# Performance work log

Measured on AMD Instinct MI355X. Metric: run time of the kernel, lower is better.

Reference implementation:

```python
import jax, jax.numpy as jnp
from jax import lax
import numpy as np

DN = ('NCDHW', 'OIDHW', 'NCDHW')
EPS = 1e-3  # BatchNorm1d eps=0.001
GRID = (41, 512, 512)  # spatial_shape [40,512,512] + [1,0,0]


def _block(x, mask, w, gamma, beta, rmean, rvar, stride, padding):
    # Regular (non-submanifold) sparse conv computes the same values as a dense
    # conv on the zero-filled grid; active OUTPUT sites are exactly those reached
    # by any active input site through the kernel window. BN+ReLU act only on
    # active sites (inactive sites stay exactly 0), hence the mask multiply.
    y = lax.conv_general_dilated(x, w, stride, padding, dimension_numbers=DN)
    k1 = jnp.ones((1, 1) + w.shape[2:], x.dtype)
    m = lax.conv_general_dilated(mask, k1, stride, padding, dimension_numbers=DN)
    m = (m > 0).astype(x.dtype)
    inv = gamma / jnp.sqrt(rvar + EPS)
    scale = inv.reshape(1, -1, 1, 1, 1)
    shift = (beta - rmean * inv).reshape(1, -1, 1, 1, 1)
    return jax.nn.relu(y * scale + shift) * m, m


def setup_inputs() -> dict:
    key = jax.random.key(0)
    NV, B = 120000, 2
    kf, kb, kz, ky, kx, kp = jax.random.split(key, 6)
    voxel_features = jax.random.normal(kf, (NV, 3), jnp.float32)
    coors = jnp.stack([
        jax.random.randint(kb, (NV,), 0, B, jnp.int32),
        jax.random.randint(kz, (NV,), 0, 40, jnp.int32),
        jax.random.randint(ky, (NV,), 0, 512, jnp.int32),
        jax.random.randint(kx, (NV,), 0, 512, jnp.int32)], axis=1)
    inp = {"voxel_features": voxel_features, "coors": coors, "batch_size": B}
    chans = [(3, 16, (3, 3, 3)), (16, 32, (3, 3, 3)), (32, 64, (3, 3, 3)), (64, 64, (3, 1, 1))]
    for i, (ci, co, k) in enumerate(chans, 1):
        kw, kg, kbb, km, kv = jax.random.split(jax.random.fold_in(kp, i), 5)
        fan = ci * k[0] * k[1] * k[2]
        inp[f"w{i}"] = jax.random.normal(kw, (co, ci) + k, jnp.float32) / np.sqrt(fan).astype(np.float32)
        inp[f"g{i}"] = jax.random.uniform(kg, (co,), jnp.float32, 0.5, 1.5)
        inp[f"bb{i}"] = jax.random.normal(kbb, (co,), jnp.float32) * 0.1
        inp[f"rm{i}"] = jax.random.normal(km, (co,), jnp.float32) * 0.1
        inp[f"rv{i}"] = jax.random.uniform(kv, (co,), jnp.float32, 0.5, 1.5)
    return inp


def reference(voxel_features, coors, batch_size,
              w1, g1, bb1, rm1, rv1,
              w2, g2, bb2, rm2, rv2,
              w3, g3, bb3, rm3, rv3,
              w4, g4, bb4, rm4, rv4):
    D, H, W = GRID
    C = voxel_features.shape[1]
    b, z, y, x = coors[:, 0], coors[:, 1], coors[:, 2], coors[:, 3]
    dense = jnp.zeros((batch_size, C, D, H, W), voxel_features.dtype)
    dense = dense.at[b, :, z, y, x].add(voxel_features)  # scatter voxels to grid
    mask = jnp.zeros((batch_size, 1, D, H, W), voxel_features.dtype).at[b, 0, z, y, x].set(1.0)
    h, m = _block(dense, mask, w1, g1, bb1, rm1, rv1, (2, 2, 2), [(1, 1), (1, 1), (1, 1)])
    h, m = _block(h, m, w2, g2, bb2, rm2, rv2, (2, 2, 2), [(1, 1), (1, 1), (1, 1)])
    h, m = _block(h, m, w3, g3, bb3, rm3, rv3, (2, 2, 2), [(0, 0), (1, 1), (1, 1)])
    h, m = _block(h, m, w4, g4, bb4, rm4, rv4, (2, 1, 1), [(0, 0), (0, 0), (0, 0)])
    N, Co, Dd, Hh, Ww = h.shape  # [B, 64, 2, 64, 64]
    return h.reshape(N, Co * Dd, Hh, Ww)
```

## Files before the change

kernel.cpp:

```cpp
#include <hip/hip_runtime.h>

#define EPS 1e-3f


static __device__ __forceinline__ unsigned f2bf(float f) {
    unsigned u = __float_as_uint(f);
    return (u + 0x7FFFu + ((u >> 16) & 1u)) >> 16;
}

typedef _Float16 f16x8 __attribute__((ext_vector_type(8)));
typedef float f32x4 __attribute__((ext_vector_type(4)));
typedef float f32x16 __attribute__((ext_vector_type(16)));

__global__ __launch_bounds__(256) void repack(
    const float* __restrict__ g1, const float* __restrict__ b1,
    const float* __restrict__ rm1, const float* __restrict__ rv1,
    const float* __restrict__ w2, const float* __restrict__ g2, const float* __restrict__ b2,
    const float* __restrict__ rm2, const float* __restrict__ rv2,
    const float* __restrict__ w3, const float* __restrict__ g3, const float* __restrict__ b3,
    const float* __restrict__ rm3, const float* __restrict__ rv3,
    const float* __restrict__ w4, const float* __restrict__ g4, const float* __restrict__ b4,
    const float* __restrict__ rm4, const float* __restrict__ rv4,
    _Float16* __restrict__ wB2, _Float16* __restrict__ wB3,
    _Float16* __restrict__ wB4, float* __restrict__ shb)
{
    const int i = blockIdx.x * 256 + threadIdx.x;
    if (i < 13824) {
        const int j = i & 7, lane = (i >> 3) & 63, tap = i >> 9;
        const int oc = lane & 31;
        const int cin = (lane >> 5) * 8 + j;
        const float inv = g2[oc] * rsqrtf(rv2[oc] + EPS);
        wB2[i] = (_Float16)(w2[(oc * 16 + cin) * 27 + tap] * inv);
    } else if (i >= 14336 && i < 69632) {
        const int j2 = i - 14336;
        const int j = j2 & 7, lane = (j2 >> 3) & 63, t = (j2 >> 9) & 3, tap = j2 >> 11;
        const int q = lane >> 4, n = lane & 15;
        const int oc = t * 16 + n;
        const int cin = q * 8 + j;
        const float inv = g3[oc] * rsqrtf(rv3[oc] + EPS);
        wB3[j2] = (_Float16)(w3[(oc * 32 + cin) * 27 + tap] * inv);
    } else if (i >= 69632 && i < 81920) {
        const int j2 = i - 69632;
        const int j = j2 & 7, lane = (j2 >> 3) & 63, t = (j2 >> 9) & 3, c = j2 >> 11;
        const int q = lane >> 4, n = lane & 15;
        const int oc = t * 16 + n;
        const int k = c * 32 + q * 8 + j;
        const int dz = k >> 6, cin = k & 63;
        const float inv = g4[oc] * rsqrtf(rv4[oc] + EPS);
        wB4[j2] = (_Float16)(w4[(oc * 64 + cin) * 3 + dz] * inv);
    } else if (i >= 81920 && i < 82112) {
        const int j = i - 81920;
        if (j < 32) {
            const float inv = g2[j] * rsqrtf(rv2[j] + EPS);
            shb[j] = b2[j] - rm2[j] * inv;
        } else if (j < 96) {
            const int o = j - 32;
            const float inv = g3[o] * rsqrtf(rv3[o] + EPS);
            shb[j] = b3[o] - rm3[o] * inv;
        } else if (j < 160) {
            const int o = j - 96;
            const float inv = g4[o] * rsqrtf(rv4[o] + EPS);
            shb[j] = b4[o] - rm4[o] * inv;
        } else if (j < 176) {
            const int o = j - 160;
            shb[j] = g1[o] * rsqrtf(rv1[o] + EPS);
        } else if (j < 192) {
            const int o = j - 176;
            const float inv = g1[o] * rsqrtf(rv1[o] + EPS);
            shb[j] = b1[o] - rm1[o] * inv;
        }
    }
}

__global__ __launch_bounds__(256) void scatter_l1(
    const float* __restrict__ vf, const int* __restrict__ coors, int NV,
    const float* __restrict__ w1, unsigned short* __restrict__ y1,
    float* __restrict__ m1)
{
    __shared__ float ws[16 * 3 * 27];
    for (int e = threadIdx.x; e < 16 * 3 * 27; e += 256) ws[e] = w1[e];
    __syncthreads();

    const int gid = blockIdx.x * 256 + threadIdx.x;
    const int i = gid >> 3;
    const int oc2 = gid & 7;
    if (i >= NV) return;
    const int oc = oc2 * 2;

    const int b = coors[4 * i + 0];
    const int z = coors[4 * i + 1];
    const int y = coors[4 * i + 2];
    const int x = coors[4 * i + 3];
    const float f0 = vf[3 * i + 0];
    const float f1 = vf[3 * i + 1];
    const float f2 = vf[3 * i + 2];

    int ozv[2], kzv[2], nz = 0;
    int oyv[2], kyv[2], ny = 0;
    int oxv[2], kxv[2], nx = 0;
#pragma unroll
    for (int k = 0; k < 3; ++k) {
        int t = z + 1 - k;
        if (t >= 0 && !(t & 1)) { int o = t >> 1; if (o < 21) { ozv[nz] = o; kzv[nz] = k; ++nz; } }
    }
#pragma unroll
    for (int k = 0; k < 3; ++k) {
        int t = y + 1 - k;
        if (t >= 0 && !(t & 1)) { int o = t >> 1; if (o < 256) { oyv[ny] = o; kyv[ny] = k; ++ny; } }
    }
#pragma unroll
    for (int k = 0; k < 3; ++k) {
        int t = x + 1 - k;
        if (t >= 0 && !(t & 1)) { int o = t >> 1; if (o < 256) { oxv[nx] = o; kxv[nx] = k; ++nx; } }
    }

    for (int a = 0; a < nz; ++a)
        for (int bb = 0; bb < ny; ++bb)
            for (int c = 0; c < nx; ++c) {
                const int oz = ozv[a], oy = oyv[bb], ox = oxv[c];
                const int tap = (kzv[a] * 3 + kyv[bb]) * 3 + kxv[c];
                const int sp = oz * 65536 + oy * 256 + ox;
                if (oc2 == 0) m1[b * 1376256 + sp] = 1.0f;
                const float s0 = ws[oc * 81 + tap] * f0 + ws[oc * 81 + 27 + tap] * f1 +
                                 ws[oc * 81 + 54 + tap] * f2;
                const float s1 = ws[(oc + 1) * 81 + tap] * f0 +
                                 ws[(oc + 1) * 81 + 27 + tap] * f1 +
                                 ws[(oc + 1) * 81 + 54 + tap] * f2;
                const unsigned pk = f2bf(s0) | (f2bf(s1) << 16);
                unsigned* addr = (unsigned*)(y1 + (size_t)(b * 1376256 + sp) * 16 +
                                             oc2 * 2);
                asm volatile("global_atomic_pk_add_bf16 %0, %1, off"
                             : : "v"(addr), "v"(pk) : "memory");
            }
}

__global__ __launch_bounds__(256) void h1_pass(
    uint4* __restrict__ y1b, const float* __restrict__ m1,
    const float* __restrict__ shb, float* __restrict__ m2)
{
    const int idx = blockIdx.x * 256 + threadIdx.x;
    const float mv = m1[idx];
    uint4 u0 = y1b[idx * 2], u1 = y1b[idx * 2 + 1];
    const unsigned d[8] = {u0.x, u0.y, u0.z, u0.w, u1.x, u1.y, u1.z, u1.w};
    unsigned o[8];
#pragma unroll
    for (int j = 0; j < 8; ++j) {
        const int c0 = 2 * j;
        const float vlo = __uint_as_float(d[j] << 16);
        const float vhi = __uint_as_float(d[j] & 0xFFFF0000u);
        const float v0 = fmaxf(vlo * shb[160 + c0] + shb[176 + c0], 0.f) * mv;
        const float v1 = fmaxf(vhi * shb[160 + c0 + 1] + shb[176 + c0 + 1], 0.f) * mv;
        o[j] = __builtin_bit_cast(unsigned, __builtin_amdgcn_cvt_pkrtz(v0, v1));
    }
    uint4 w0, w1;
    w0.x = o[0]; w0.y = o[1]; w0.z = o[2]; w0.w = o[3];
    w1.x = o[4]; w1.y = o[5]; w1.z = o[6]; w1.w = o[7];
    y1b[idx * 2] = w0;
    y1b[idx * 2 + 1] = w1;

    if (idx < 360448) {
        const int b = idx / 180224;
        const int r = idx - b * 180224;
        const int oz = r >> 14, r2 = r & 16383, oy = r2 >> 7, ox = r2 & 127;
        const int iz0 = 2 * oz - 1, iyb = 2 * oy - 1, ixb = 2 * ox - 1;
        float msum = 0.f;
#pragma unroll
        for (int kz = 0; kz < 3; ++kz) {
            const int iz = iz0 + kz;
#pragma unroll
            for (int ky = 0; ky < 3; ++ky) {
                const int iy = iyb + ky;
#pragma unroll
                for (int kx = 0; kx < 3; ++kx) {
                    const int ix = ixb + kx;
                    if ((unsigned)iz < 21u && (unsigned)iy < 256u &&
                        (unsigned)ix < 256u)
                        msum += m1[b * 1376256 + iz * 65536 + iy * 256 + ix];
                }
            }
        }
        m2[idx] = msum > 0.f ? 1.f : 0.f;
    }
}

__global__ __launch_bounds__(256) void build_m3(
    const float* __restrict__ m2, float* __restrict__ m3)
{
    const int idx = blockIdx.x * 256 + threadIdx.x;
    if (idx >= 40960) return;
    const int b = idx / 20480;
    const int r = idx - b * 20480;
    const int oz = r >> 12, r2 = r & 4095, oy = r2 >> 6, ox = r2 & 63;
    const int iz0 = 2 * oz, iyb = 2 * oy - 1, ixb = 2 * ox - 1;

    float msum = 0.f;
#pragma unroll
    for (int kz = 0; kz < 3; ++kz) {
        const int iz = iz0 + kz;
#pragma unroll
        for (int ky = 0; ky < 3; ++ky) {
            const int iy = iyb + ky;
#pragma unroll
            for (int kx = 0; kx < 3; ++kx) {
                const int ix = ixb + kx;
                if ((unsigned)iy < 128u && (unsigned)ix < 128u)
                    msum += m2[b * 180224 + iz * 16384 + iy * 128 + ix];
            }
        }
    }
    m3[idx] = msum > 0.f ? 1.f : 0.f;
}

__global__ __launch_bounds__(256) __attribute__((amdgpu_waves_per_eu(4, 8)))
void conv_l2(
    const unsigned char* __restrict__ h1,
    const uint4* __restrict__ wB2,
    const float* __restrict__ m2, const float* __restrict__ shb,
    _Float16* __restrict__ h2h)
{
    const int tid = threadIdx.x;
    const int gw = blockIdx.x * 4 + (tid >> 6);
    const int lane = tid & 63;
    const int m = lane & 31, h = lane >> 5;

    const int plane = gw >> 9;
    const int rem = gw & 511;
    const int oy = rem >> 2;
    const int ox0 = (rem & 3) * 32;
    const int b = plane / 11, oz = plane % 11;
    const int iz0 = 2 * oz - 1, iyb = 2 * oy - 1;
    const int ixm = 2 * (ox0 + m) - 1;
    const int bbase = b * 1376256;
    const int qoff = h * 16;

    f32x16 acc;
#pragma unroll
    for (int r = 0; r < 16; ++r) acc[r] = 0.f;

    uint4 buf[13];
    bool  val[13];
#pragma unroll
    for (int t = 0; t < 13; ++t) {
        const int kz = t / 9, ky = (t / 3) % 3, kx = t % 3;
        const int iz = iz0 + kz, iy = iyb + ky, ix = ixm + kx;
        const bool v = (unsigned)iz < 21u && (unsigned)iy < 256u &&
                       (unsigned)ix < 256u;
        const int cell = bbase + iz * 65536 + iy * 256 + ix;
        buf[t] = *(const uint4*)(h1 + (v ? (cell * 32 + qoff) : 0));
        val[t] = v;
    }

#pragma unroll
    for (int tap = 0; tap < 27; ++tap) {
        const int s = tap % 13;
        uint4 ua = buf[s];
        if (!val[s]) { ua.x = 0; ua.y = 0; ua.z = 0; ua.w = 0; }
        if (tap + 13 < 27) {
            const int t2 = tap + 13;
            const int kz = t2 / 9, ky = (t2 / 3) % 3, kx = t2 % 3;
            const int iz = iz0 + kz, iy = iyb + ky, ix = ixm + kx;
            const bool v = (unsigned)iz < 21u && (unsigned)iy < 256u &&
                           (unsigned)ix < 256u;
            const int cell = bbase + iz * 65536 + iy * 256 + ix;
            buf[s] = *(const uint4*)(h1 + (v ? (cell * 32 + qoff) : 0));
            val[s] = v;
        }
        const f16x8 af = __builtin_bit_cast(f16x8, ua);
        const f16x8 bf = __builtin_bit_cast(f16x8, wB2[tap * 64 + lane]);
        acc = __builtin_amdgcn_mfma_f32_32x32x16_f16(af, bf, acc, 0, 0, 0);
    }

    const int oc = lane & 31;
#pragma unroll
    for (int r = 0; r < 16; ++r) {
        const int row = (r & 3) + 8 * (r >> 2) + 4 * h;
        const int px = ox0 + row;
        const int spo = oz * 16384 + oy * 128 + px;
        const float mv = m2[b * 180224 + spo];
        const size_t cbase = (size_t)(b * 180224 + spo) * 32;
        h2h[cbase + oc] = (_Float16)(fmaxf(acc[r] + shb[oc], 0.f) * mv);
    }
}

__global__ __launch_bounds__(256) __attribute__((amdgpu_waves_per_eu(4, 8)))
void conv_l3(
    const unsigned char* __restrict__ h2h,
    const uint4* __restrict__ wB3,
    const float* __restrict__ m3, const float* __restrict__ shb,
    _Float16* __restrict__ h3h)
{
    const int tid = threadIdx.x;
    const int gw = blockIdx.x * 4 + (tid >> 6);
    const int lane = tid & 63;
    const int m = lane & 15, q = lane >> 4;

    const int plane = gw >> 8;
    const int rem = gw & 255;
    const int oy = rem >> 2;
    const int ox0 = (rem & 3) * 16;
    const int b = plane / 5, oz = plane % 5;
    const int iz0 = 2 * oz, iyb = 2 * oy - 1;
    const int ixm = 2 * (ox0 + m) - 1;
    const int bbase = b * 180224;
    const int qoff = q * 16;

    f32x4 acc[4];
#pragma unroll
    for (int t = 0; t < 4; ++t) acc[t] = (f32x4){0.f, 0.f, 0.f, 0.f};

    uint4 buf[9];
    bool  val[9];
#pragma unroll
    for (int t = 0; t < 9; ++t) {
        const int ky = (t / 3) % 3, kx = t % 3;
        const int iz = iz0 + t / 9, iy = iyb + ky, ix = ixm + kx;
        const bool v = (unsigned)iy < 128u && (unsigned)ix < 128u;
        const int cell = bbase + iz * 16384 + iy * 128 + ix;
        buf[t] = *(const uint4*)(h2h + (v ? (cell * 64 + qoff) : 0));
        val[t] = v;
    }

#pragma unroll
    for (int tap = 0; tap < 27; ++tap) {
        const int s = tap % 9;
        uint4 ua = buf[s];
        if (!val[s]) { ua.x = 0; ua.y = 0; ua.z = 0; ua.w = 0; }
        if (tap + 9 < 27) {
            const int t2 = tap + 9;
            const int kz = t2 / 9, ky = (t2 / 3) % 3, kx = t2 % 3;
            const int iz = iz0 + kz, iy = iyb + ky, ix = ixm + kx;
            const bool v = (unsigned)iy < 128u && (unsigned)ix < 128u;
            const int cell = bbase + iz * 16384 + iy * 128 + ix;
            buf[s] = *(const uint4*)(h2h + (v ? (cell * 64 + qoff) : 0));
            val[s] = v;
        }
        const f16x8 af = __builtin_bit_cast(f16x8, ua);
#pragma unroll
        for (int t = 0; t < 4; ++t) {
            const f16x8 bf = __builtin_bit_cast(f16x8, wB3[(tap * 4 + t) * 64 + lane]);
            acc[t] = __builtin_amdgcn_mfma_f32_16x16x32_f16(af, bf, acc[t], 0, 0, 0);
        }
    }

    const int n = lane & 15;
#pragma unroll
    for (int r = 0; r < 4; ++r) {
        const int px = ox0 + q * 4 + r;
        const int spo = oz * 4096 + oy * 64 + px;
        const float mv = m3[b * 20480 + spo];
        const size_t cb = (size_t)(b * 20480 + spo) * 64;
#pragma unroll
        for (int t = 0; t < 4; ++t) {
            const int oc = t * 16 + n;
            h3h[cb + oc] = (_Float16)(fmaxf(acc[t][r] + shb[32 + oc], 0.f) * mv);
        }
    }
}

__global__ __launch_bounds__(256) __attribute__((amdgpu_waves_per_eu(4, 8)))
void conv_l4(
    const unsigned char* __restrict__ h3h,
    const uint4* __restrict__ wB4,
    const float* __restrict__ m3, const float* __restrict__ shb,
    float* __restrict__ out)
{
    const int tid = threadIdx.x;
    const int gw = blockIdx.x * 4 + (tid >> 6);
    const int lane = tid & 63;
    const int m = lane & 15, q = lane >> 4;

    const int b = gw >> 9, od = (gw >> 8) & 1;
    const int oy = (gw >> 2) & 63, ox0 = (gw & 3) * 16;
    const int cellbase = (b * 5 + 2 * od) * 4096 + oy * 64 + ox0 + m;

    f32x4 acc[4];
#pragma unroll
    for (int t = 0; t < 4; ++t) acc[t] = (f32x4){0.f, 0.f, 0.f, 0.f};

#pragma unroll
    for (int c = 0; c < 6; ++c) {
        const int dz = c >> 1;
        const size_t addr = (size_t)(cellbase + dz * 4096) * 128 +
                            (c & 1) * 64 + q * 16;
        const uint4 ua = *(const uint4*)(h3h + addr);
        const f16x8 af = __builtin_bit_cast(f16x8, ua);
#pragma unroll
        for (int t = 0; t < 4; ++t) {
            const f16x8 bf = __builtin_bit_cast(f16x8, wB4[(c * 4 + t) * 64 + lane]);
            acc[t] = __builtin_amdgcn_mfma_f32_16x16x32_f16(af, bf, acc[t], 0, 0, 0);
        }
    }

    const int n = lane & 15;
#pragma unroll
    for (int r = 0; r < 4; ++r) {
        const int px = ox0 + q * 4 + r;
        const int spo = oy * 64 + px;
        const float msum = m3[(b * 5 + 2 * od + 0) * 4096 + spo] +
                           m3[(b * 5 + 2 * od + 1) * 4096 + spo] +
                           m3[(b * 5 + 2 * od + 2) * 4096 + spo];
        const float mv = msum > 0.f ? 1.f : 0.f;
#pragma unroll
        for (int t = 0; t < 4; ++t) {
            const int oc = t * 16 + n;
            out[((b * 64 + oc) * 2 + od) * 4096 + spo] =
                fmaxf(acc[t][r] + shb[96 + oc], 0.f) * mv;
        }
    }
}

extern "C" void kernel_launch(void* const* d_in, const int* in_sizes, int n_in,
                              void* d_out, int out_size, void* d_ws, size_t ws_size,
                              hipStream_t stream)
{
    const float* vf    = (const float*)d_in[0];
    const int*   coors = (const int*)d_in[1];
    const float* w1 = (const float*)d_in[3];
    const float* g1 = (const float*)d_in[4];
    const float* b1 = (const float*)d_in[5];
    const float* rm1 = (const float*)d_in[6];
    const float* rv1 = (const float*)d_in[7];
    const float* w2 = (const float*)d_in[8];
    const float* g2 = (const float*)d_in[9];
    const float* b2 = (const float*)d_in[10];
    const float* rm2 = (const float*)d_in[11];
    const float* rv2 = (const float*)d_in[12];
    const float* w3 = (const float*)d_in[13];
    const float* g3 = (const float*)d_in[14];
    const float* b3 = (const float*)d_in[15];
    const float* rm3 = (const float*)d_in[16];
    const float* rv3 = (const float*)d_in[17];
    const float* w4 = (const float*)d_in[18];
    const float* g4 = (const float*)d_in[19];
    const float* b4 = (const float*)d_in[20];
    const float* rm4 = (const float*)d_in[21];
    const float* rv4 = (const float*)d_in[22];

    const int NV = in_sizes[0] / 3;

    float* ws = (float*)d_ws;
    float* y1  = ws;
    float* m1  = y1 + 22020096;
    float* h2h = m1 + 2752512;
    float* m2  = h2h + 5767168;
    float* h3h = m2 + 360448;
    float* m3  = h3h + 1310720;
    float* wB2 = m3 + 40960;
    float* wB3 = wB2 + 7168;
    float* wB4 = wB3 + 27648;
    float* shb = wB4 + 6144;

    (void)hipMemsetAsync(y1, 0, (size_t)(22020096 + 2752512) * sizeof(float), stream);

    repack<<<321, 256, 0, stream>>>(g1, b1, rm1, rv1,
                                    w2, g2, b2, rm2, rv2, w3, g3, b3, rm3, rv3,
                                    w4, g4, b4, rm4, rv4,
                                    (_Float16*)wB2, (_Float16*)wB3,
                                    (_Float16*)wB4, shb);
    scatter_l1<<<(NV * 8 + 255) / 256, 256, 0, stream>>>(vf, coors, NV, w1,
                                                         (unsigned short*)y1, m1);
    h1_pass<<<10752, 256, 0, stream>>>((uint4*)y1, m1, shb, m2);
    build_m3<<<160, 256, 0, stream>>>(m2, m3);
    conv_l2<<<2816, 256, 0, stream>>>((const unsigned char*)y1, (const uint4*)wB2,
                                      m2, shb, (_Float16*)h2h);
    conv_l3<<<640, 256, 0, stream>>>((const unsigned char*)h2h, (const uint4*)wB3,
                                     m3, shb, (_Float16*)h3h);
    conv_l4<<<256, 256, 0, stream>>>((const unsigned char*)h3h, (const uint4*)wB4,
                                     m3, shb, (float*)d_out);
}
```

Baseline: 238.3 us.

## Replace full-grid memset with sparse prezero and byte mask for layer one

```diff
diff --git a/kernel.cpp b/kernel.cpp
--- a/kernel.cpp
+++ b/kernel.cpp
@@ -12,7 +12,7 @@
 typedef float f32x4 __attribute__((ext_vector_type(4)));
 typedef float f32x16 __attribute__((ext_vector_type(16)));
 
-__global__ __launch_bounds__(256) void repack(
+__global__ __launch_bounds__(256) void repack_prezero(
     const float* __restrict__ g1, const float* __restrict__ b1,
     const float* __restrict__ rm1, const float* __restrict__ rv1,
     const float* __restrict__ w2, const float* __restrict__ g2, const float* __restrict__ b2,
@@ -22,8 +22,46 @@
     const float* __restrict__ w4, const float* __restrict__ g4, const float* __restrict__ b4,
     const float* __restrict__ rm4, const float* __restrict__ rv4,
     _Float16* __restrict__ wB2, _Float16* __restrict__ wB3,
-    _Float16* __restrict__ wB4, float* __restrict__ shb)
-{
+    _Float16* __restrict__ wB4, float* __restrict__ shb,
+    const int* __restrict__ coors, int NV, unsigned short* __restrict__ y1)
+{
+    if (blockIdx.x >= 321) {
+        const int i = (blockIdx.x - 321) * 256 + threadIdx.x;
+        if (i < NV) {
+            const int b = coors[4 * i + 0];
+            const int z = coors[4 * i + 1];
+            const int y = coors[4 * i + 2];
+            const int x = coors[4 * i + 3];
+            int ozv[2], nz = 0, oyv[2], ny = 0, oxv[2], nx = 0;
+#pragma unroll
+            for (int k = 0; k < 3; ++k) {
+                int t = z + 1 - k;
+                if (t >= 0 && !(t & 1)) { int o = t >> 1; if (o < 21) ozv[nz++] = o; }
+            }
+#pragma unroll
+            for (int k = 0; k < 3; ++k) {
+                int t = y + 1 - k;
+                if (t >= 0 && !(t & 1)) { int o = t >> 1; if (o < 256) oyv[ny++] = o; }
+            }
+#pragma unroll
+            for (int k = 0; k < 3; ++k) {
+                int t = x + 1 - k;
+                if (t >= 0 && !(t & 1)) { int o = t >> 1; if (o < 256) oxv[nx++] = o; }
+            }
+            const uint4 zz = {0u, 0u, 0u, 0u};
+            for (int a = 0; a < nz; ++a)
+                for (int bb = 0; bb < ny; ++bb)
+                    for (int c = 0; c < nx; ++c) {
+                        const int sp = ozv[a] * 65536 + oyv[bb] * 256 + oxv[c];
+                        uint4* p = (uint4*)(y1 + (size_t)(b * 1376256 + sp) * 16);
+                        p[0] = zz;
+                        p[1] = zz;
+                    }
+        }
+        asm volatile("s_waitcnt vmcnt(0)" ::: "memory");
+        return;
+    }
+
     const int i = blockIdx.x * 256 + threadIdx.x;
     if (i < 13824) {
         const int j = i & 7, lane = (i >> 3) & 63, tap = i >> 9;
@@ -74,96 +112,104 @@
 
 __global__ __launch_bounds__(256) void scatter_l1(
     const float* __restrict__ vf, const int* __restrict__ coors, int NV,
-    const float* __restrict__ w1, unsigned short* __restrict__ y1,
-    float* __restrict__ m1)
+    const float* __restrict__ w1, const float* __restrict__ shb,
+    unsigned short* __restrict__ y1, unsigned char* __restrict__ m1)
 {
     __shared__ float ws[16 * 3 * 27];
-    for (int e = threadIdx.x; e < 16 * 3 * 27; e += 256) ws[e] = w1[e];
+    for (int e = threadIdx.x; e < 16 * 3 * 27; e += 256)
+        ws[e] = w1[e] * shb[160 + e / 81];
     __syncthreads();
 
     const int gid = blockIdx.x * 256 + threadIdx.x;
     const int i = gid >> 3;
     const int oc2 = gid & 7;
-    if (i >= NV) return;
-    const int oc = oc2 * 2;
-
-    const int b = coors[4 * i + 0];
-    const int z = coors[4 * i + 1];
-    const int y = coors[4 * i + 2];
-    const int x = coors[4 * i + 3];
-    const float f0 = vf[3 * i + 0];
-    const float f1 = vf[3 * i + 1];
-    const float f2 = vf[3 * i + 2];
-
-    int ozv[2], kzv[2], nz = 0;
-    int oyv[2], kyv[2], ny = 0;
-    int oxv[2], kxv[2], nx = 0;
-#pragma unroll
-    for (int k = 0; k < 3; ++k) {
-        int t = z + 1 - k;
-        if (t >= 0 && !(t & 1)) { int o = t >> 1; if (o < 21) { ozv[nz] = o; kzv[nz] = k; ++nz; } }
-    }
-#pragma unroll
-    for (int k = 0; k < 3; ++k) {
-        int t = y + 1 - k;
-        if (t >= 0 && !(t & 1)) { int o = t >> 1; if (o < 256) { oyv[ny] = o; kyv[ny] = k; ++ny; } }
-    }
-#pragma unroll
-    for (int k = 0; k < 3; ++k) {
-        int t = x + 1 - k;
-        if (t >= 0 && !(t & 1)) { int o = t >> 1; if (o < 256) { oxv[nx] = o; kxv[nx] = k; ++nx; } }
-    }
-
-    for (int a = 0; a < nz; ++a)
-        for (int bb = 0; bb < ny; ++bb)
-            for (int c = 0; c < nx; ++c) {
-                const int oz = ozv[a], oy = oyv[bb], ox = oxv[c];
-                const int tap = (kzv[a] * 3 + kyv[bb]) * 3 + kxv[c];
-                const int sp = oz * 65536 + oy * 256 + ox;
-                if (oc2 == 0) m1[b * 1376256 + sp] = 1.0f;
-                const float s0 = ws[oc * 81 + tap] * f0 + ws[oc * 81 + 27 + tap] * f1 +
-                                 ws[oc * 81 + 54 + tap] * f2;
-                const float s1 = ws[(oc + 1) * 81 + tap] * f0 +
-                                 ws[(oc + 1) * 81 + 27 + tap] * f1 +
-                                 ws[(oc + 1) * 81 + 54 + tap] * f2;
-                const unsigned pk = f2bf(s0) | (f2bf(s1) << 16);
-                unsigned* addr = (unsigned*)(y1 + (size_t)(b * 1376256 + sp) * 16 +
-                                             oc2 * 2);
-                asm volatile("global_atomic_pk_add_bf16 %0, %1, off"
-                             : : "v"(addr), "v"(pk) : "memory");
-            }
+    if (i < NV) {
+        const int oc = oc2 * 2;
+
+        const int b = coors[4 * i + 0];
+        const int z = coors[4 * i + 1];
+        const int y = coors[4 * i + 2];
+        const int x = coors[4 * i + 3];
+        const float f0 = vf[3 * i + 0];
+        const float f1 = vf[3 * i + 1];
+        const float f2 = vf[3 * i + 2];
+
+        int ozv[2], kzv[2], nz = 0;
+        int oyv[2], kyv[2], ny = 0;
+        int oxv[2], kxv[2], nx = 0;
+#pragma unroll
+        for (int k = 0; k < 3; ++k) {
+            int t = z + 1 - k;
+            if (t >= 0 && !(t & 1)) { int o = t >> 1; if (o < 21) { ozv[nz] = o; kzv[nz] = k; ++nz; } }
+        }
+#pragma unroll
+        for (int k = 0; k < 3; ++k) {
+            int t = y + 1 - k;
+            if (t >= 0 && !(t & 1)) { int o = t >> 1; if (o < 256) { oyv[ny] = o; kyv[ny] = k; ++ny; } }
+        }
+#pragma unroll
+        for (int k = 0; k < 3; ++k) {
+            int t = x + 1 - k;
+            if (t >= 0 && !(t & 1)) { int o = t >> 1; if (o < 256) { oxv[nx] = o; kxv[nx] = k; ++nx; } }
+        }
+
+        for (int a = 0; a < nz; ++a)
+            for (int bb = 0; bb < ny; ++bb)
+                for (int c = 0; c < nx; ++c) {
+                    const int oz = ozv[a], oy = oyv[bb], ox = oxv[c];
+                    const int tap = (kzv[a] * 3 + kyv[bb]) * 3 + kxv[c];
+                    const int sp = oz * 65536 + oy * 256 + ox;
+                    if (oc2 == 0) m1[b * 1376256 + sp] = 1;
+                    const float s0 = ws[oc * 81 + tap] * f0 + ws[oc * 81 + 27 + tap] * f1 +
+                                     ws[oc * 81 + 54 + tap] * f2;
+                    const float s1 = ws[(oc + 1) * 81 + tap] * f0 +
+                                     ws[(oc + 1) * 81 + 27 + tap] * f1 +
+                                     ws[(oc + 1) * 81 + 54 + tap] * f2;
+                    const unsigned pk = f2bf(s0) | (f2bf(s1) << 16);
+                    unsigned* addr = (unsigned*)(y1 + (size_t)(b * 1376256 + sp) * 16 +
+                                                 oc2 * 2);
+                    asm volatile("global_atomic_pk_add_bf16 %0, %1, off"
+                                 : : "v"(addr), "v"(pk) : "memory");
+                }
+    }
+    asm volatile("s_waitcnt vmcnt(0)" ::: "memory");
 }
 
 __global__ __launch_bounds__(256) void h1_pass(
-    uint4* __restrict__ y1b, const float* __restrict__ m1,
+    uint4* __restrict__ y1b, const unsigned char* __restrict__ m1,
     const float* __restrict__ shb, float* __restrict__ m2)
 {
     const int idx = blockIdx.x * 256 + threadIdx.x;
-    const float mv = m1[idx];
-    uint4 u0 = y1b[idx * 2], u1 = y1b[idx * 2 + 1];
-    const unsigned d[8] = {u0.x, u0.y, u0.z, u0.w, u1.x, u1.y, u1.z, u1.w};
-    unsigned o[8];
-#pragma unroll
-    for (int j = 0; j < 8; ++j) {
-        const int c0 = 2 * j;
-        const float vlo = __uint_as_float(d[j] << 16);
-        const float vhi = __uint_as_float(d[j] & 0xFFFF0000u);
-        const float v0 = fmaxf(vlo * shb[160 + c0] + shb[176 + c0], 0.f) * mv;
-        const float v1 = fmaxf(vhi * shb[160 + c0 + 1] + shb[176 + c0 + 1], 0.f) * mv;
-        o[j] = __builtin_bit_cast(unsigned, __builtin_amdgcn_cvt_pkrtz(v0, v1));
-    }
-    uint4 w0, w1;
-    w0.x = o[0]; w0.y = o[1]; w0.z = o[2]; w0.w = o[3];
-    w1.x = o[4]; w1.y = o[5]; w1.z = o[6]; w1.w = o[7];
-    y1b[idx * 2] = w0;
-    y1b[idx * 2 + 1] = w1;
+    if (m1[idx]) {
+        uint4 u0 = y1b[idx * 2], u1 = y1b[idx * 2 + 1];
+        const unsigned d[8] = {u0.x, u0.y, u0.z, u0.w, u1.x, u1.y, u1.z, u1.w};
+        unsigned o[8];
+#pragma unroll
+        for (int j = 0; j < 8; ++j) {
+            const int c0 = 2 * j;
+            const float vlo = __uint_as_float(d[j] << 16);
+            const float vhi = __uint_as_float(d[j] & 0xFFFF0000u);
+            const float v0 = fmaxf(vlo + shb[176 + c0], 0.f);
+            const float v1 = fmaxf(vhi + shb[176 + c0 + 1], 0.f);
+            o[j] = __builtin_bit_cast(unsigned, __builtin_amdgcn_cvt_pkrtz(v0, v1));
+        }
+        uint4 w0, w1;
+        w0.x = o[0]; w0.y = o[1]; w0.z = o[2]; w0.w = o[3];
+        w1.x = o[4]; w1.y = o[5]; w1.z = o[6]; w1.w = o[7];
+        y1b[idx * 2] = w0;
+        y1b[idx * 2 + 1] = w1;
+    } else {
+        const uint4 zz = {0u, 0u, 0u, 0u};
+        y1b[idx * 2] = zz;
+        y1b[idx * 2 + 1] = zz;
+    }
 
     if (idx < 360448) {
         const int b = idx / 180224;
         const int r = idx - b * 180224;
         const int oz = r >> 14, r2 = r & 16383, oy = r2 >> 7, ox = r2 & 127;
         const int iz0 = 2 * oz - 1, iyb = 2 * oy - 1, ixb = 2 * ox - 1;
-        float msum = 0.f;
+        unsigned msum = 0;
 #pragma unroll
         for (int kz = 0; kz < 3; ++kz) {
             const int iz = iz0 + kz;
@@ -175,11 +221,11 @@
                     const int ix = ixb + kx;
                     if ((unsigned)iz < 21u && (unsigned)iy < 256u &&
                         (unsigned)ix < 256u)
-                        msum += m1[b * 1376256 + iz * 65536 + iy * 256 + ix];
+                        msum |= m1[b * 1376256 + iz * 65536 + iy * 256 + ix];
                 }
             }
         }
-        m2[idx] = msum > 0.f ? 1.f : 0.f;
+        m2[idx] = msum ? 1.f : 0.f;
     }
 }
 
@@ -440,8 +486,8 @@
 
     float* ws = (float*)d_ws;
     float* y1  = ws;
-    float* m1  = y1 + 22020096;
-    float* h2h = m1 + 2752512;
+    float* m1f = y1 + 22020096;
+    float* h2h = m1f + 2752512;
     float* m2  = h2h + 5767168;
     float* h3h = m2 + 360448;
     float* m3  = h3h + 1310720;
@@ -450,14 +496,18 @@
     float* wB4 = wB3 + 27648;
     float* shb = wB4 + 6144;
 
-    (void)hipMemsetAsync(y1, 0, (size_t)(22020096 + 2752512) * sizeof(float), stream);
-
-    repack<<<321, 256, 0, stream>>>(g1, b1, rm1, rv1,
-                                    w2, g2, b2, rm2, rv2, w3, g3, b3, rm3, rv3,
-                                    w4, g4, b4, rm4, rv4,
-                                    (_Float16*)wB2, (_Float16*)wB3,
-                                    (_Float16*)wB4, shb);
-    scatter_l1<<<(NV * 8 + 255) / 256, 256, 0, stream>>>(vf, coors, NV, w1,
+    unsigned char* m1 = (unsigned char*)m1f;
+
+    (void)hipMemsetAsync(m1, 0, 2752512, stream);
+
+    const int pzBlocks = (NV + 255) / 256;
+    repack_prezero<<<321 + pzBlocks, 256, 0, stream>>>(
+        g1, b1, rm1, rv1,
+        w2, g2, b2, rm2, rv2, w3, g3, b3, rm3, rv3,
+        w4, g4, b4, rm4, rv4,
+        (_Float16*)wB2, (_Float16*)wB3, (_Float16*)wB4, shb,
+        coors, NV, (unsigned short*)y1);
+    scatter_l1<<<(NV * 8 + 255) / 256, 256, 0, stream>>>(vf, coors, NV, w1, shb,
                                                          (unsigned short*)y1, m1);
     h1_pass<<<10752, 256, 0, stream>>>((uint4*)y1, m1, shb, m2);
     build_m3<<<160, 256, 0, stream>>>(m2, m3);
```

Result: faster. 225.8 us (-5.2%).
